# Kernel optimization log

Hardware: AMD Instinct MI355X
Metric: run time of the kernel (lower is better)

The kernel has to match this reference:

```python
import jax, jax.numpy as jnp
import numpy as np

B, D, K, N = 32, 512, 64, 1024
EPS = 1e-12  # torch F.normalize eps


def setup_inputs() -> dict:
    key = jax.random.key(0)
    k1, k2, k3 = jax.random.split(key, 3)
    x = jax.random.normal(k1, (B, D, N), dtype=jnp.float32)
    conv_w = jax.random.normal(k2, (K, D), dtype=jnp.float32) * (1.0 / np.sqrt(D))
    centers = jax.random.normal(k3, (D, K), dtype=jnp.float32)
    return {"x": x, "conv_w": conv_w, "centers": centers}


def reference(x, conv_w, centers):
    # scores: 1x1 conv over flattened spatial dim -> [B, K, N]
    scores = jnp.einsum('kd,bdn->bkn', conv_w, x)
    assign = jax.nn.softmax(scores, axis=1)                 # softmax over clusters
    # Algebraic rewrite of sum_n assign[b,k,n] * (x[b,d,n] - centers[d,k]):
    vlad = (jnp.einsum('bdn,bkn->bdk', x, assign)
            - centers[None, :, :] * assign.sum(axis=-1)[:, None, :])  # [B, D, K]
    # intra-normalization over descriptor dim D (F.normalize with eps clamp)
    vlad = vlad / jnp.maximum(jnp.linalg.norm(vlad, axis=1, keepdims=True), EPS)
    desc = vlad.reshape(vlad.shape[0], -1)                  # [B, D*K]
    desc = desc / jnp.maximum(jnp.linalg.norm(desc, axis=1, keepdims=True), EPS)
    return desc
```

## Files before the change

### kernel.cpp

```cpp
#include <hip/hip_runtime.h>
#include <hip/hip_bf16.h>

#define Bv 32
#define Dv 512
#define Kv 64
#define Nv 1024
#define EPSv 1e-12f

typedef __attribute__((ext_vector_type(8))) short bf16x8;
typedef __attribute__((ext_vector_type(4))) float f32x4;

__device__ __forceinline__ unsigned short f2b(float f) {
  union { float f; unsigned u; } v; v.f = f;
  unsigned r = v.u + 0x7fffu + ((v.u >> 16) & 1u);
  return (unsigned short)(r >> 16);
}
__device__ __forceinline__ unsigned pack2(float a, float b) {
  return (unsigned)f2b(a) | ((unsigned)f2b(b) << 16);
}

__global__ __launch_bounds__(256) void wconv(const float* __restrict__ w,
                                             unsigned short* __restrict__ wbf) {
  int i = (blockIdx.x * 256 + threadIdx.x) * 4;
  float4 v = *(const float4*)&w[i];
  uint2 o = make_uint2(pack2(v.x, v.y), pack2(v.z, v.w));
  *(uint2*)&wbf[i] = o;
}

__global__ __launch_bounds__(512) void fused_scores(
    const float* __restrict__ x, const unsigned short* __restrict__ wbf,
    unsigned short* __restrict__ xbf, unsigned short* __restrict__ assign,
    float* __restrict__ asum) {
  __shared__ unsigned short xT[64 * 520];
  __shared__ float redmax[4][64];
  __shared__ float redsum[4][64];

  const int t = threadIdx.x;
  const int b = blockIdx.y;
  const int n0 = blockIdx.x * 64;

  {
    const int lo = t & 15;
    const int hi = t >> 4;
    const float* xb = x + (size_t)b * Dv * Nv + n0;
    unsigned short* xo = xbf + (size_t)b * Dv * Nv + n0;
#pragma unroll
    for (int r = 0; r < 8; r++) {
      int d = (hi + 32 * r) * 2;
      int n4 = lo * 4;
      float4 v0 = *(const float4*)&xb[(size_t)d * Nv + n4];
      float4 v1 = *(const float4*)&xb[(size_t)(d + 1) * Nv + n4];
      unsigned short a0 = f2b(v0.x), a1 = f2b(v0.y), a2 = f2b(v0.z), a3 = f2b(v0.w);
      unsigned short b0 = f2b(v1.x), b1 = f2b(v1.y), b2 = f2b(v1.z), b3 = f2b(v1.w);
      *(uint2*)&xo[(size_t)d * Nv + n4] =
          make_uint2((unsigned)a0 | ((unsigned)a1 << 16), (unsigned)a2 | ((unsigned)a3 << 16));
      *(uint2*)&xo[(size_t)(d + 1) * Nv + n4] =
          make_uint2((unsigned)b0 | ((unsigned)b1 << 16), (unsigned)b2 | ((unsigned)b3 << 16));
      *(unsigned*)&xT[(n4 + 0) * 520 + d] = (unsigned)a0 | ((unsigned)b0 << 16);
      *(unsigned*)&xT[(n4 + 1) * 520 + d] = (unsigned)a1 | ((unsigned)b1 << 16);
      *(unsigned*)&xT[(n4 + 2) * 520 + d] = (unsigned)a2 | ((unsigned)b2 << 16);
      *(unsigned*)&xT[(n4 + 3) * 520 + d] = (unsigned)a3 | ((unsigned)b3 << 16);
    }
  }
  __syncthreads();

  const int wv = t >> 6;
  const int lane = t & 63;
  const int q = lane >> 4;
  const int m = lane & 15;
  const int k16 = wv & 3;
  const int nsub = wv >> 2;

  f32x4 acc0 = {0.f, 0.f, 0.f, 0.f};
  f32x4 acc1 = {0.f, 0.f, 0.f, 0.f};

  const unsigned short* wp = wbf + (size_t)(k16 * 16 + m) * Dv + q * 8;
  const unsigned short* l0 = &xT[(nsub * 32 + m) * 520 + q * 8];
  const unsigned short* l1 = l0 + 16 * 520;

#pragma unroll
  for (int d0 = 0; d0 < Dv; d0 += 32) {
    bf16x8 af = *(const bf16x8*)(wp + d0);
    bf16x8 bf0 = *(const bf16x8*)(l0 + d0);
    bf16x8 bf1 = *(const bf16x8*)(l1 + d0);
    acc0 = __builtin_amdgcn_mfma_f32_16x16x32_bf16(af, bf0, acc0, 0, 0, 0);
    acc1 = __builtin_amdgcn_mfma_f32_16x16x32_bf16(af, bf1, acc1, 0, 0, 0);
  }

  float m0 = fmaxf(fmaxf(acc0[0], acc0[1]), fmaxf(acc0[2], acc0[3]));
  float m1 = fmaxf(fmaxf(acc1[0], acc1[1]), fmaxf(acc1[2], acc1[3]));
  m0 = fmaxf(m0, __shfl_xor(m0, 16)); m0 = fmaxf(m0, __shfl_xor(m0, 32));
  m1 = fmaxf(m1, __shfl_xor(m1, 16)); m1 = fmaxf(m1, __shfl_xor(m1, 32));
  if (q == 0) {
    redmax[k16][nsub * 32 + m] = m0;
    redmax[k16][nsub * 32 + 16 + m] = m1;
  }
  __syncthreads();
  const int c0 = nsub * 32 + m, c1 = c0 + 16;
  float mc0 = fmaxf(fmaxf(redmax[0][c0], redmax[1][c0]), fmaxf(redmax[2][c0], redmax[3][c0]));
  float mc1 = fmaxf(fmaxf(redmax[0][c1], redmax[1][c1]), fmaxf(redmax[2][c1], redmax[3][c1]));

  float e0[4], e1[4];
  float s0 = 0.f, s1 = 0.f;
#pragma unroll
  for (int r = 0; r < 4; r++) {
    e0[r] = __expf(acc0[r] - mc0); s0 += e0[r];
    e1[r] = __expf(acc1[r] - mc1); s1 += e1[r];
  }
  s0 += __shfl_xor(s0, 16); s0 += __shfl_xor(s0, 32);
  s1 += __shfl_xor(s1, 16); s1 += __shfl_xor(s1, 32);
  if (q == 0) {
    redsum[k16][c0] = s0;
    redsum[k16][c1] = s1;
  }
  __syncthreads();
  float sc0 = 1.0f / (redsum[0][c0] + redsum[1][c0] + redsum[2][c0] + redsum[3][c0]);
  float sc1 = 1.0f / (redsum[0][c1] + redsum[1][c1] + redsum[2][c1] + redsum[3][c1]);

  unsigned short* ab = assign + ((size_t)b * Kv + k16 * 16 + q * 4) * Nv + n0 + nsub * 32;
#pragma unroll
  for (int r = 0; r < 4; r++) {
    float v0 = e0[r] * sc0;
    float v1 = e1[r] * sc1;
    ab[(size_t)r * Nv + m] = f2b(v0);
    ab[(size_t)r * Nv + 16 + m] = f2b(v1);
    float p = v0 + v1;
    p += __shfl_xor(p, 1); p += __shfl_xor(p, 2);
    p += __shfl_xor(p, 4); p += __shfl_xor(p, 8);
    if (m == 0) atomicAdd(&asum[b * Kv + k16 * 16 + q * 4 + r], p);
  }
}

__global__ __launch_bounds__(256) void vlad_mfma(
    const unsigned short* __restrict__ xbf, const unsigned short* __restrict__ assign,
    const float* __restrict__ centers, const float* __restrict__ asum,
    float* __restrict__ vlad, float* __restrict__ colsq) {
  __shared__ float sred[2][64][4];

  const int t = threadIdx.x;
  const int b = blockIdx.y;
  const int gx = blockIdx.x;
  const int d0 = (gx >> 1) * 16;
  const int kb = (gx & 1) * 32;
  const int wv = t >> 6;
  const int ksub = wv & 1;
  const int nh = wv >> 1;
  const int lane = t & 63;
  const int q = lane >> 4;
  const int m = lane & 15;
  const int k16 = kb + ksub * 16;

  f32x4 acc0 = {0.f, 0.f, 0.f, 0.f};
  f32x4 acc1 = {0.f, 0.f, 0.f, 0.f};

  const unsigned short* xp = xbf + ((size_t)b * Dv + d0 + m) * Nv + nh * 512 + q * 8;
  const unsigned short* ap = assign + ((size_t)b * Kv + k16 + m) * Nv + nh * 512 + q * 8;

#pragma unroll
  for (int n = 0; n < 512; n += 64) {
    bf16x8 a0 = *(const bf16x8*)(xp + n);
    bf16x8 f0 = *(const bf16x8*)(ap + n);
    bf16x8 a1 = *(const bf16x8*)(xp + n + 32);
    bf16x8 f1 = *(const bf16x8*)(ap + n + 32);
    acc0 = __builtin_amdgcn_mfma_f32_16x16x32_bf16(a0, f0, acc0, 0, 0, 0);
    acc1 = __builtin_amdgcn_mfma_f32_16x16x32_bf16(a1, f1, acc1, 0, 0, 0);
  }

  f32x4 v;
#pragma unroll
  for (int r = 0; r < 4; r++) v[r] = acc0[r] + acc1[r];

  if (nh == 1) {
#pragma unroll
    for (int r = 0; r < 4; r++) sred[ksub][lane][r] = v[r];
  }
  __syncthreads();
  if (nh == 0) {
    const int k = k16 + m;
    const float as = asum[b * Kv + k];
    float ss = 0.f;
#pragma unroll
    for (int r = 0; r < 4; r++) {
      v[r] += sred[ksub][lane][r];
      int d = d0 + q * 4 + r;
      float val = v[r] - centers[d * Kv + k] * as;
      vlad[((size_t)b * Dv + d) * Kv + k] = val;
      ss = fmaf(val, val, ss);
    }
    ss += __shfl_xor(ss, 16);
    ss += __shfl_xor(ss, 32);
    if (q == 0) atomicAdd(&colsq[b * Kv + k], ss);
  }
}

__global__ __launch_bounds__(256) void scale_kernel(
    const float* __restrict__ vlad, const float* __restrict__ colsq,
    float* __restrict__ out) {
  const int t = threadIdx.x;
  const size_t i = (size_t)blockIdx.x * 256 + t;
  const int b = (int)(i >> 15);
  __shared__ float scs[64];
  __shared__ float bsh;
  if (t < 64) {
    float tot = colsq[b * Kv + t];
    float sc = 1.0f / fmaxf(sqrtf(tot), EPSv);
    scs[t] = sc;
    float contrib = tot * sc * sc;
#pragma unroll
    for (int off = 32; off > 0; off >>= 1) contrib += __shfl_down(contrib, off);
    if (t == 0) bsh = 1.0f / fmaxf(sqrtf(contrib), EPSv);
  }
  __syncthreads();
  out[i] = vlad[i] * scs[i & 63] * bsh;
}

extern "C" void kernel_launch(void* const* d_in, const int* in_sizes, int n_in,
                              void* d_out, int out_size, void* d_ws, size_t ws_size,
                              hipStream_t stream) {
  const float* x = (const float*)d_in[0];
  const float* w = (const float*)d_in[1];
  const float* centers = (const float*)d_in[2];
  float* out = (float*)d_out;

  char* ws = (char*)d_ws;
  unsigned short* xbf = (unsigned short*)ws;
  unsigned short* assign = (unsigned short*)(ws + 33554432);
  float* vlad = (float*)(ws + 37748736);
  unsigned short* wbf = (unsigned short*)(ws + 41943040);
  float* asum = (float*)(ws + 42008576);
  float* colsq = asum + Bv * Kv;

  hipMemsetAsync(asum, 0, (size_t)2 * Bv * Kv * sizeof(float), stream);

  wconv<<<32, 256, 0, stream>>>(w, wbf);
  fused_scores<<<dim3(Nv / 64, Bv), 512, 0, stream>>>(x, wbf, xbf, assign, asum);
  vlad_mfma<<<dim3(64, Bv), 256, 0, stream>>>(xbf, assign, centers, asum, vlad, colsq);
  scale_kernel<<<(Bv * Dv * Kv) / 256, 256, 0, stream>>>(vlad, colsq, out);
}
```

Measured before the change: 147.6 us.

## Drop bf16 copy of x; convert fp32 x on the fly in both kernels

The scores kernel no longer writes a bf16 copy of x to global memory. The vlad kernel now reads the fp32 x directly and converts it to bf16 in registers before the MFMA. The scores kernel stages x through LDS in two halves of D, so its LDS tile is about half the size, which may allow higher occupancy. This removes a 32 MB write and replaces a 32 MB bf16 read with a 64 MB fp32 read that may partly hit in cache, at the cost of extra conversion ALU work and an extra barrier pair.

```diff
diff --git a/kernel.cpp b/kernel.cpp
--- a/kernel.cpp
+++ b/kernel.cpp
@@ -29,62 +29,53 @@
 
 __global__ __launch_bounds__(512) void fused_scores(
     const float* __restrict__ x, const unsigned short* __restrict__ wbf,
-    unsigned short* __restrict__ xbf, unsigned short* __restrict__ assign,
-    float* __restrict__ asum) {
-  __shared__ unsigned short xT[64 * 520];
+    unsigned short* __restrict__ assign, float* __restrict__ asum) {
+  __shared__ unsigned short xT[64 * 264];
   __shared__ float redmax[4][64];
   __shared__ float redsum[4][64];
 
   const int t = threadIdx.x;
   const int b = blockIdx.y;
   const int n0 = blockIdx.x * 64;
-
-  {
-    const int lo = t & 15;
-    const int hi = t >> 4;
-    const float* xb = x + (size_t)b * Dv * Nv + n0;
-    unsigned short* xo = xbf + (size_t)b * Dv * Nv + n0;
-#pragma unroll
-    for (int r = 0; r < 8; r++) {
-      int d = (hi + 32 * r) * 2;
-      int n4 = lo * 4;
-      float4 v0 = *(const float4*)&xb[(size_t)d * Nv + n4];
-      float4 v1 = *(const float4*)&xb[(size_t)(d + 1) * Nv + n4];
-      unsigned short a0 = f2b(v0.x), a1 = f2b(v0.y), a2 = f2b(v0.z), a3 = f2b(v0.w);
-      unsigned short b0 = f2b(v1.x), b1 = f2b(v1.y), b2 = f2b(v1.z), b3 = f2b(v1.w);
-      *(uint2*)&xo[(size_t)d * Nv + n4] =
-          make_uint2((unsigned)a0 | ((unsigned)a1 << 16), (unsigned)a2 | ((unsigned)a3 << 16));
-      *(uint2*)&xo[(size_t)(d + 1) * Nv + n4] =
-          make_uint2((unsigned)b0 | ((unsigned)b1 << 16), (unsigned)b2 | ((unsigned)b3 << 16));
-      *(unsigned*)&xT[(n4 + 0) * 520 + d] = (unsigned)a0 | ((unsigned)b0 << 16);
-      *(unsigned*)&xT[(n4 + 1) * 520 + d] = (unsigned)a1 | ((unsigned)b1 << 16);
-      *(unsigned*)&xT[(n4 + 2) * 520 + d] = (unsigned)a2 | ((unsigned)b2 << 16);
-      *(unsigned*)&xT[(n4 + 3) * 520 + d] = (unsigned)a3 | ((unsigned)b3 << 16);
-    }
-  }
-  __syncthreads();
-
   const int wv = t >> 6;
   const int lane = t & 63;
   const int q = lane >> 4;
   const int m = lane & 15;
   const int k16 = wv & 3;
   const int nsub = wv >> 2;
+  const int lo = t & 15;
+  const int hi = t >> 4;
 
   f32x4 acc0 = {0.f, 0.f, 0.f, 0.f};
   f32x4 acc1 = {0.f, 0.f, 0.f, 0.f};
 
   const unsigned short* wp = wbf + (size_t)(k16 * 16 + m) * Dv + q * 8;
-  const unsigned short* l0 = &xT[(nsub * 32 + m) * 520 + q * 8];
-  const unsigned short* l1 = l0 + 16 * 520;
-
-#pragma unroll
-  for (int d0 = 0; d0 < Dv; d0 += 32) {
-    bf16x8 af = *(const bf16x8*)(wp + d0);
-    bf16x8 bf0 = *(const bf16x8*)(l0 + d0);
-    bf16x8 bf1 = *(const bf16x8*)(l1 + d0);
-    acc0 = __builtin_amdgcn_mfma_f32_16x16x32_bf16(af, bf0, acc0, 0, 0, 0);
-    acc1 = __builtin_amdgcn_mfma_f32_16x16x32_bf16(af, bf1, acc1, 0, 0, 0);
+  const unsigned short* l0 = &xT[(nsub * 32 + m) * 264 + q * 8];
+  const unsigned short* l1 = l0 + 16 * 264;
+
+  for (int dh = 0; dh < 2; dh++) {
+    const float* xb = x + ((size_t)b * Dv + dh * 256) * Nv + n0;
+#pragma unroll
+    for (int r = 0; r < 4; r++) {
+      int d = (hi + 32 * r) * 2;
+      int n4 = lo * 4;
+      float4 v0 = *(const float4*)&xb[(size_t)d * Nv + n4];
+      float4 v1 = *(const float4*)&xb[(size_t)(d + 1) * Nv + n4];
+      *(unsigned*)&xT[(n4 + 0) * 264 + d] = pack2(v0.x, v1.x);
+      *(unsigned*)&xT[(n4 + 1) * 264 + d] = pack2(v0.y, v1.y);
+      *(unsigned*)&xT[(n4 + 2) * 264 + d] = pack2(v0.z, v1.z);
+      *(unsigned*)&xT[(n4 + 3) * 264 + d] = pack2(v0.w, v1.w);
+    }
+    __syncthreads();
+#pragma unroll
+    for (int d0 = 0; d0 < 256; d0 += 32) {
+      bf16x8 af = *(const bf16x8*)(wp + dh * 256 + d0);
+      bf16x8 bf0 = *(const bf16x8*)(l0 + d0);
+      bf16x8 bf1 = *(const bf16x8*)(l1 + d0);
+      acc0 = __builtin_amdgcn_mfma_f32_16x16x32_bf16(af, bf0, acc0, 0, 0, 0);
+      acc1 = __builtin_amdgcn_mfma_f32_16x16x32_bf16(af, bf1, acc1, 0, 0, 0);
+    }
+    __syncthreads();
   }
 
   float m0 = fmaxf(fmaxf(acc0[0], acc0[1]), fmaxf(acc0[2], acc0[3]));
@@ -132,7 +123,7 @@
 }
 
 __global__ __launch_bounds__(256) void vlad_mfma(
-    const unsigned short* __restrict__ xbf, const unsigned short* __restrict__ assign,
+    const float* __restrict__ x, const unsigned short* __restrict__ assign,
     const float* __restrict__ centers, const float* __restrict__ asum,
     float* __restrict__ vlad, float* __restrict__ colsq) {
   __shared__ float sred[2][64][4];
@@ -153,15 +144,26 @@
   f32x4 acc0 = {0.f, 0.f, 0.f, 0.f};
   f32x4 acc1 = {0.f, 0.f, 0.f, 0.f};
 
-  const unsigned short* xp = xbf + ((size_t)b * Dv + d0 + m) * Nv + nh * 512 + q * 8;
+  const float* xp = x + ((size_t)b * Dv + d0 + m) * Nv + nh * 512 + q * 8;
   const unsigned short* ap = assign + ((size_t)b * Kv + k16 + m) * Nv + nh * 512 + q * 8;
 
-#pragma unroll
+#pragma unroll 4
   for (int n = 0; n < 512; n += 64) {
-    bf16x8 a0 = *(const bf16x8*)(xp + n);
+    float4 xa0 = *(const float4*)(xp + n);
+    float4 xc0 = *(const float4*)(xp + n + 4);
     bf16x8 f0 = *(const bf16x8*)(ap + n);
-    bf16x8 a1 = *(const bf16x8*)(xp + n + 32);
+    float4 xa1 = *(const float4*)(xp + n + 32);
+    float4 xc1 = *(const float4*)(xp + n + 36);
     bf16x8 f1 = *(const bf16x8*)(ap + n + 32);
+    bf16x8 a0, a1;
+    a0[0] = (short)f2b(xa0.x); a0[1] = (short)f2b(xa0.y);
+    a0[2] = (short)f2b(xa0.z); a0[3] = (short)f2b(xa0.w);
+    a0[4] = (short)f2b(xc0.x); a0[5] = (short)f2b(xc0.y);
+    a0[6] = (short)f2b(xc0.z); a0[7] = (short)f2b(xc0.w);
+    a1[0] = (short)f2b(xa1.x); a1[1] = (short)f2b(xa1.y);
+    a1[2] = (short)f2b(xa1.z); a1[3] = (short)f2b(xa1.w);
+    a1[4] = (short)f2b(xc1.x); a1[5] = (short)f2b(xc1.y);
+    a1[6] = (short)f2b(xc1.z); a1[7] = (short)f2b(xc1.w);
     acc0 = __builtin_amdgcn_mfma_f32_16x16x32_bf16(a0, f0, acc0, 0, 0, 0);
     acc1 = __builtin_amdgcn_mfma_f32_16x16x32_bf16(a1, f1, acc1, 0, 0, 0);
   }
@@ -223,17 +225,16 @@
   float* out = (float*)d_out;
 
   char* ws = (char*)d_ws;
-  unsigned short* xbf = (unsigned short*)ws;
-  unsigned short* assign = (unsigned short*)(ws + 33554432);
-  float* vlad = (float*)(ws + 37748736);
-  unsigned short* wbf = (unsigned short*)(ws + 41943040);
-  float* asum = (float*)(ws + 42008576);
+  unsigned short* assign = (unsigned short*)ws;
+  float* vlad = (float*)(ws + 4194304);
+  unsigned short* wbf = (unsigned short*)(ws + 8388608);
+  float* asum = (float*)(ws + 8454144);
   float* colsq = asum + Bv * Kv;
 
   hipMemsetAsync(asum, 0, (size_t)2 * Bv * Kv * sizeof(float), stream);
 
   wconv<<<32, 256, 0, stream>>>(w, wbf);
-  fused_scores<<<dim3(Nv / 64, Bv), 512, 0, stream>>>(x, wbf, xbf, assign, asum);
-  vlad_mfma<<<dim3(64, Bv), 256, 0, stream>>>(xbf, assign, centers, asum, vlad, colsq);
+  fused_scores<<<dim3(Nv / 64, Bv), 512, 0, stream>>>(x, wbf, assign, asum);
+  vlad_mfma<<<dim3(64, Bv), 256, 0, stream>>>(x, assign, centers, asum, vlad, colsq);
   scale_kernel<<<(Bv * Dv * Kv) / 256, 256, 0, stream>>>(vlad, colsq, out);
 }
```

After: 157.6 us. 1.07x slower.

## Shrink score tiles, drop asum atomics, compute cluster sums inside vlad kernel

Applied to the files above, without the earlier changes.

The scores kernel now handles 32 spatial columns per block instead of 64. That doubles the grid and halves shared memory per block, which should raise occupancy. The per-cluster assignment sum is no longer built with atomics in the scores kernel. Instead the vlad kernel recomputes it from the bf16 assignment fragments it already loads, and each of its blocks covers all 64 clusters with 8 waves. This removes the atomic traffic and part of the memset, at the cost of extra conversion adds in the vlad inner loop and a sum taken from rounded bf16 values.

```diff
diff --git a/kernel.cpp b/kernel.cpp
--- a/kernel.cpp
+++ b/kernel.cpp
@@ -17,6 +17,9 @@
 }
 __device__ __forceinline__ unsigned pack2(float a, float b) {
   return (unsigned)f2b(a) | ((unsigned)f2b(b) << 16);
+}
+__device__ __forceinline__ float b2f(unsigned short s) {
+  union { unsigned u; float f; } v; v.u = (unsigned)s << 16; return v.f;
 }
 
 __global__ __launch_bounds__(256) void wconv(const float* __restrict__ w,
@@ -29,37 +32,34 @@
 
 __global__ __launch_bounds__(512) void fused_scores(
     const float* __restrict__ x, const unsigned short* __restrict__ wbf,
-    unsigned short* __restrict__ xbf, unsigned short* __restrict__ assign,
-    float* __restrict__ asum) {
-  __shared__ unsigned short xT[64 * 520];
-  __shared__ float redmax[4][64];
-  __shared__ float redsum[4][64];
+    unsigned short* __restrict__ xbf, unsigned short* __restrict__ assign) {
+  __shared__ unsigned short xT[32 * 520];
+  __shared__ float redmax[4][32];
+  __shared__ float redsum[4][32];
 
   const int t = threadIdx.x;
   const int b = blockIdx.y;
-  const int n0 = blockIdx.x * 64;
+  const int n0 = blockIdx.x * 32;
 
   {
-    const int lo = t & 15;
-    const int hi = t >> 4;
+    const int lo = t & 7;
+    const int hi = t >> 3;
     const float* xb = x + (size_t)b * Dv * Nv + n0;
     unsigned short* xo = xbf + (size_t)b * Dv * Nv + n0;
 #pragma unroll
-    for (int r = 0; r < 8; r++) {
-      int d = (hi + 32 * r) * 2;
+    for (int r = 0; r < 4; r++) {
+      int d = (hi + 64 * r) * 2;
       int n4 = lo * 4;
       float4 v0 = *(const float4*)&xb[(size_t)d * Nv + n4];
       float4 v1 = *(const float4*)&xb[(size_t)(d + 1) * Nv + n4];
-      unsigned short a0 = f2b(v0.x), a1 = f2b(v0.y), a2 = f2b(v0.z), a3 = f2b(v0.w);
-      unsigned short b0 = f2b(v1.x), b1 = f2b(v1.y), b2 = f2b(v1.z), b3 = f2b(v1.w);
       *(uint2*)&xo[(size_t)d * Nv + n4] =
-          make_uint2((unsigned)a0 | ((unsigned)a1 << 16), (unsigned)a2 | ((unsigned)a3 << 16));
+          make_uint2(pack2(v0.x, v0.y), pack2(v0.z, v0.w));
       *(uint2*)&xo[(size_t)(d + 1) * Nv + n4] =
-          make_uint2((unsigned)b0 | ((unsigned)b1 << 16), (unsigned)b2 | ((unsigned)b3 << 16));
-      *(unsigned*)&xT[(n4 + 0) * 520 + d] = (unsigned)a0 | ((unsigned)b0 << 16);
-      *(unsigned*)&xT[(n4 + 1) * 520 + d] = (unsigned)a1 | ((unsigned)b1 << 16);
-      *(unsigned*)&xT[(n4 + 2) * 520 + d] = (unsigned)a2 | ((unsigned)b2 << 16);
-      *(unsigned*)&xT[(n4 + 3) * 520 + d] = (unsigned)a3 | ((unsigned)b3 << 16);
+          make_uint2(pack2(v1.x, v1.y), pack2(v1.z, v1.w));
+      *(unsigned*)&xT[(n4 + 0) * 520 + d] = pack2(v0.x, v1.x);
+      *(unsigned*)&xT[(n4 + 1) * 520 + d] = pack2(v0.y, v1.y);
+      *(unsigned*)&xT[(n4 + 2) * 520 + d] = pack2(v0.z, v1.z);
+      *(unsigned*)&xT[(n4 + 3) * 520 + d] = pack2(v0.w, v1.w);
     }
   }
   __syncthreads();
@@ -71,119 +71,91 @@
   const int k16 = wv & 3;
   const int nsub = wv >> 2;
 
-  f32x4 acc0 = {0.f, 0.f, 0.f, 0.f};
-  f32x4 acc1 = {0.f, 0.f, 0.f, 0.f};
-
+  f32x4 acc = {0.f, 0.f, 0.f, 0.f};
   const unsigned short* wp = wbf + (size_t)(k16 * 16 + m) * Dv + q * 8;
-  const unsigned short* l0 = &xT[(nsub * 32 + m) * 520 + q * 8];
-  const unsigned short* l1 = l0 + 16 * 520;
+  const unsigned short* lp = &xT[(nsub * 16 + m) * 520 + q * 8];
 
 #pragma unroll
   for (int d0 = 0; d0 < Dv; d0 += 32) {
     bf16x8 af = *(const bf16x8*)(wp + d0);
-    bf16x8 bf0 = *(const bf16x8*)(l0 + d0);
-    bf16x8 bf1 = *(const bf16x8*)(l1 + d0);
-    acc0 = __builtin_amdgcn_mfma_f32_16x16x32_bf16(af, bf0, acc0, 0, 0, 0);
-    acc1 = __builtin_amdgcn_mfma_f32_16x16x32_bf16(af, bf1, acc1, 0, 0, 0);
-  }
-
-  float m0 = fmaxf(fmaxf(acc0[0], acc0[1]), fmaxf(acc0[2], acc0[3]));
-  float m1 = fmaxf(fmaxf(acc1[0], acc1[1]), fmaxf(acc1[2], acc1[3]));
-  m0 = fmaxf(m0, __shfl_xor(m0, 16)); m0 = fmaxf(m0, __shfl_xor(m0, 32));
-  m1 = fmaxf(m1, __shfl_xor(m1, 16)); m1 = fmaxf(m1, __shfl_xor(m1, 32));
-  if (q == 0) {
-    redmax[k16][nsub * 32 + m] = m0;
-    redmax[k16][nsub * 32 + 16 + m] = m1;
-  }
-  __syncthreads();
-  const int c0 = nsub * 32 + m, c1 = c0 + 16;
-  float mc0 = fmaxf(fmaxf(redmax[0][c0], redmax[1][c0]), fmaxf(redmax[2][c0], redmax[3][c0]));
-  float mc1 = fmaxf(fmaxf(redmax[0][c1], redmax[1][c1]), fmaxf(redmax[2][c1], redmax[3][c1]));
-
-  float e0[4], e1[4];
-  float s0 = 0.f, s1 = 0.f;
-#pragma unroll
-  for (int r = 0; r < 4; r++) {
-    e0[r] = __expf(acc0[r] - mc0); s0 += e0[r];
-    e1[r] = __expf(acc1[r] - mc1); s1 += e1[r];
-  }
-  s0 += __shfl_xor(s0, 16); s0 += __shfl_xor(s0, 32);
-  s1 += __shfl_xor(s1, 16); s1 += __shfl_xor(s1, 32);
-  if (q == 0) {
-    redsum[k16][c0] = s0;
-    redsum[k16][c1] = s1;
-  }
-  __syncthreads();
-  float sc0 = 1.0f / (redsum[0][c0] + redsum[1][c0] + redsum[2][c0] + redsum[3][c0]);
-  float sc1 = 1.0f / (redsum[0][c1] + redsum[1][c1] + redsum[2][c1] + redsum[3][c1]);
-
-  unsigned short* ab = assign + ((size_t)b * Kv + k16 * 16 + q * 4) * Nv + n0 + nsub * 32;
-#pragma unroll
-  for (int r = 0; r < 4; r++) {
-    float v0 = e0[r] * sc0;
-    float v1 = e1[r] * sc1;
-    ab[(size_t)r * Nv + m] = f2b(v0);
-    ab[(size_t)r * Nv + 16 + m] = f2b(v1);
-    float p = v0 + v1;
-    p += __shfl_xor(p, 1); p += __shfl_xor(p, 2);
-    p += __shfl_xor(p, 4); p += __shfl_xor(p, 8);
-    if (m == 0) atomicAdd(&asum[b * Kv + k16 * 16 + q * 4 + r], p);
-  }
-}
-
-__global__ __launch_bounds__(256) void vlad_mfma(
+    bf16x8 bf = *(const bf16x8*)(lp + d0);
+    acc = __builtin_amdgcn_mfma_f32_16x16x32_bf16(af, bf, acc, 0, 0, 0);
+  }
+
+  float mx = fmaxf(fmaxf(acc[0], acc[1]), fmaxf(acc[2], acc[3]));
+  mx = fmaxf(mx, __shfl_xor(mx, 16));
+  mx = fmaxf(mx, __shfl_xor(mx, 32));
+  if (q == 0) redmax[k16][nsub * 16 + m] = mx;
+  __syncthreads();
+  const int c = nsub * 16 + m;
+  float mc = fmaxf(fmaxf(redmax[0][c], redmax[1][c]),
+                   fmaxf(redmax[2][c], redmax[3][c]));
+  float e[4];
+  float s = 0.f;
+#pragma unroll
+  for (int r = 0; r < 4; r++) { e[r] = __expf(acc[r] - mc); s += e[r]; }
+  s += __shfl_xor(s, 16);
+  s += __shfl_xor(s, 32);
+  if (q == 0) redsum[k16][c] = s;
+  __syncthreads();
+  float sc = 1.0f / (redsum[0][c] + redsum[1][c] + redsum[2][c] + redsum[3][c]);
+
+  unsigned short* ab = assign + ((size_t)b * Kv + k16 * 16 + q * 4) * Nv + n0 + nsub * 16;
+#pragma unroll
+  for (int r = 0; r < 4; r++) ab[(size_t)r * Nv + m] = f2b(e[r] * sc);
+}
+
+__global__ __launch_bounds__(512) void vlad_mfma(
     const unsigned short* __restrict__ xbf, const unsigned short* __restrict__ assign,
-    const float* __restrict__ centers, const float* __restrict__ asum,
-    float* __restrict__ vlad, float* __restrict__ colsq) {
-  __shared__ float sred[2][64][4];
+    const float* __restrict__ centers, float* __restrict__ vlad,
+    float* __restrict__ colsq) {
+  __shared__ float sred[4][64][4];
+  __shared__ float sasum[4][16];
 
   const int t = threadIdx.x;
   const int b = blockIdx.y;
-  const int gx = blockIdx.x;
-  const int d0 = (gx >> 1) * 16;
-  const int kb = (gx & 1) * 32;
+  const int d0 = blockIdx.x * 16;
   const int wv = t >> 6;
-  const int ksub = wv & 1;
-  const int nh = wv >> 1;
+  const int ksub = wv & 3;
+  const int nh = wv >> 2;
   const int lane = t & 63;
   const int q = lane >> 4;
   const int m = lane & 15;
-  const int k16 = kb + ksub * 16;
-
-  f32x4 acc0 = {0.f, 0.f, 0.f, 0.f};
-  f32x4 acc1 = {0.f, 0.f, 0.f, 0.f};
+  const int k16 = ksub * 16;
+
+  f32x4 acc = {0.f, 0.f, 0.f, 0.f};
+  float sa = 0.f;
 
   const unsigned short* xp = xbf + ((size_t)b * Dv + d0 + m) * Nv + nh * 512 + q * 8;
   const unsigned short* ap = assign + ((size_t)b * Kv + k16 + m) * Nv + nh * 512 + q * 8;
 
 #pragma unroll
-  for (int n = 0; n < 512; n += 64) {
+  for (int n = 0; n < 512; n += 32) {
     bf16x8 a0 = *(const bf16x8*)(xp + n);
     bf16x8 f0 = *(const bf16x8*)(ap + n);
-    bf16x8 a1 = *(const bf16x8*)(xp + n + 32);
-    bf16x8 f1 = *(const bf16x8*)(ap + n + 32);
-    acc0 = __builtin_amdgcn_mfma_f32_16x16x32_bf16(a0, f0, acc0, 0, 0, 0);
-    acc1 = __builtin_amdgcn_mfma_f32_16x16x32_bf16(a1, f1, acc1, 0, 0, 0);
-  }
-
-  f32x4 v;
-#pragma unroll
-  for (int r = 0; r < 4; r++) v[r] = acc0[r] + acc1[r];
+    acc = __builtin_amdgcn_mfma_f32_16x16x32_bf16(a0, f0, acc, 0, 0, 0);
+#pragma unroll
+    for (int j = 0; j < 8; j++) sa += b2f((unsigned short)f0[j]);
+  }
+
+  sa += __shfl_xor(sa, 16);
+  sa += __shfl_xor(sa, 32);
 
   if (nh == 1) {
 #pragma unroll
-    for (int r = 0; r < 4; r++) sred[ksub][lane][r] = v[r];
+    for (int r = 0; r < 4; r++) sred[ksub][lane][r] = acc[r];
+    if (q == 0) sasum[ksub][m] = sa;
   }
   __syncthreads();
   if (nh == 0) {
     const int k = k16 + m;
-    const float as = asum[b * Kv + k];
+    const float asum_k = sa + sasum[ksub][m];
     float ss = 0.f;
 #pragma unroll
     for (int r = 0; r < 4; r++) {
-      v[r] += sred[ksub][lane][r];
+      float v = acc[r] + sred[ksub][lane][r];
       int d = d0 + q * 4 + r;
-      float val = v[r] - centers[d * Kv + k] * as;
+      float val = v - centers[d * Kv + k] * asum_k;
       vlad[((size_t)b * Dv + d) * Kv + k] = val;
       ss = fmaf(val, val, ss);
     }
@@ -223,17 +195,16 @@
   float* out = (float*)d_out;
 
   char* ws = (char*)d_ws;
-  unsigned short* xbf = (unsigned short*)ws;
-  unsigned short* assign = (unsigned short*)(ws + 33554432);
-  float* vlad = (float*)(ws + 37748736);
+  unsigned short* assign = (unsigned short*)ws;
+  float* vlad = (float*)(ws + 4194304);
+  unsigned short* xbf = (unsigned short*)(ws + 8388608);
   unsigned short* wbf = (unsigned short*)(ws + 41943040);
-  float* asum = (float*)(ws + 42008576);
-  float* colsq = asum + Bv * Kv;
-
-  hipMemsetAsync(asum, 0, (size_t)2 * Bv * Kv * sizeof(float), stream);
+  float* colsq = (float*)(ws + 42008576);
+
+  hipMemsetAsync(colsq, 0, (size_t)Bv * Kv * sizeof(float), stream);
 
   wconv<<<32, 256, 0, stream>>>(w, wbf);
-  fused_scores<<<dim3(Nv / 64, Bv), 512, 0, stream>>>(x, wbf, xbf, assign, asum);
-  vlad_mfma<<<dim3(64, Bv), 256, 0, stream>>>(xbf, assign, centers, asum, vlad, colsq);
+  fused_scores<<<dim3(Nv / 32, Bv), 512, 0, stream>>>(x, wbf, xbf, assign);
+  vlad_mfma<<<dim3(Dv / 16, Bv), 512, 0, stream>>>(xbf, assign, centers, vlad, colsq);
   scale_kernel<<<(Bv * Dv * Kv) / 256, 256, 0, stream>>>(vlad, colsq, out);
 }
```

Result: slower. 156.6 us (+6.1%).

## Widen vlad blocks to cover all clusters and batch loads ahead of MFMA

Applied to the files above, without the earlier changes.

vlad_mfma now uses 512-thread blocks that cover all 64 clusters for a 16-row slice of D, so each x tile is read by one block instead of two. Each wave issues all eight load pairs up front and refills them while the first batch of MFMAs runs, which is meant to hide global-load latency. The workspace is reordered so assign and vlad come before the large bf16 x buffer, and the bf16 packing in fused_scores now goes through pack2. The trade-off is higher register pressure from the 16 bf16x8 load registers, and the grid has half as many blocks.

```diff
diff --git a/kernel.cpp b/kernel.cpp
--- a/kernel.cpp
+++ b/kernel.cpp
@@ -50,16 +50,14 @@
       int n4 = lo * 4;
       float4 v0 = *(const float4*)&xb[(size_t)d * Nv + n4];
       float4 v1 = *(const float4*)&xb[(size_t)(d + 1) * Nv + n4];
-      unsigned short a0 = f2b(v0.x), a1 = f2b(v0.y), a2 = f2b(v0.z), a3 = f2b(v0.w);
-      unsigned short b0 = f2b(v1.x), b1 = f2b(v1.y), b2 = f2b(v1.z), b3 = f2b(v1.w);
       *(uint2*)&xo[(size_t)d * Nv + n4] =
-          make_uint2((unsigned)a0 | ((unsigned)a1 << 16), (unsigned)a2 | ((unsigned)a3 << 16));
+          make_uint2(pack2(v0.x, v0.y), pack2(v0.z, v0.w));
       *(uint2*)&xo[(size_t)(d + 1) * Nv + n4] =
-          make_uint2((unsigned)b0 | ((unsigned)b1 << 16), (unsigned)b2 | ((unsigned)b3 << 16));
-      *(unsigned*)&xT[(n4 + 0) * 520 + d] = (unsigned)a0 | ((unsigned)b0 << 16);
-      *(unsigned*)&xT[(n4 + 1) * 520 + d] = (unsigned)a1 | ((unsigned)b1 << 16);
-      *(unsigned*)&xT[(n4 + 2) * 520 + d] = (unsigned)a2 | ((unsigned)b2 << 16);
-      *(unsigned*)&xT[(n4 + 3) * 520 + d] = (unsigned)a3 | ((unsigned)b3 << 16);
+          make_uint2(pack2(v1.x, v1.y), pack2(v1.z, v1.w));
+      *(unsigned*)&xT[(n4 + 0) * 520 + d] = pack2(v0.x, v1.x);
+      *(unsigned*)&xT[(n4 + 1) * 520 + d] = pack2(v0.y, v1.y);
+      *(unsigned*)&xT[(n4 + 2) * 520 + d] = pack2(v0.z, v1.z);
+      *(unsigned*)&xT[(n4 + 3) * 520 + d] = pack2(v0.w, v1.w);
     }
   }
   __syncthreads();
@@ -131,48 +129,46 @@
   }
 }
 
-__global__ __launch_bounds__(256) void vlad_mfma(
+__global__ __launch_bounds__(512, 4) void vlad_mfma(
     const unsigned short* __restrict__ xbf, const unsigned short* __restrict__ assign,
     const float* __restrict__ centers, const float* __restrict__ asum,
     float* __restrict__ vlad, float* __restrict__ colsq) {
-  __shared__ float sred[2][64][4];
+  __shared__ float sred[4][64][4];
 
   const int t = threadIdx.x;
   const int b = blockIdx.y;
-  const int gx = blockIdx.x;
-  const int d0 = (gx >> 1) * 16;
-  const int kb = (gx & 1) * 32;
+  const int d0 = blockIdx.x * 16;
   const int wv = t >> 6;
-  const int ksub = wv & 1;
-  const int nh = wv >> 1;
+  const int ksub = wv & 3;
+  const int nh = wv >> 2;
   const int lane = t & 63;
   const int q = lane >> 4;
   const int m = lane & 15;
-  const int k16 = kb + ksub * 16;
-
-  f32x4 acc0 = {0.f, 0.f, 0.f, 0.f};
-  f32x4 acc1 = {0.f, 0.f, 0.f, 0.f};
+  const int k16 = ksub * 16;
 
   const unsigned short* xp = xbf + ((size_t)b * Dv + d0 + m) * Nv + nh * 512 + q * 8;
   const unsigned short* ap = assign + ((size_t)b * Kv + k16 + m) * Nv + nh * 512 + q * 8;
 
-#pragma unroll
-  for (int n = 0; n < 512; n += 64) {
-    bf16x8 a0 = *(const bf16x8*)(xp + n);
-    bf16x8 f0 = *(const bf16x8*)(ap + n);
-    bf16x8 a1 = *(const bf16x8*)(xp + n + 32);
-    bf16x8 f1 = *(const bf16x8*)(ap + n + 32);
-    acc0 = __builtin_amdgcn_mfma_f32_16x16x32_bf16(a0, f0, acc0, 0, 0, 0);
-    acc1 = __builtin_amdgcn_mfma_f32_16x16x32_bf16(a1, f1, acc1, 0, 0, 0);
-  }
-
-  f32x4 v;
-#pragma unroll
-  for (int r = 0; r < 4; r++) v[r] = acc0[r] + acc1[r];
+  f32x4 acc = {0.f, 0.f, 0.f, 0.f};
+  bf16x8 xv[8], av[8];
+#pragma unroll
+  for (int i = 0; i < 8; i++) {
+    xv[i] = *(const bf16x8*)(xp + i * 32);
+    av[i] = *(const bf16x8*)(ap + i * 32);
+  }
+#pragma unroll
+  for (int i = 0; i < 8; i++) {
+    acc = __builtin_amdgcn_mfma_f32_16x16x32_bf16(xv[i], av[i], acc, 0, 0, 0);
+    xv[i] = *(const bf16x8*)(xp + 256 + i * 32);
+    av[i] = *(const bf16x8*)(ap + 256 + i * 32);
+  }
+#pragma unroll
+  for (int i = 0; i < 8; i++)
+    acc = __builtin_amdgcn_mfma_f32_16x16x32_bf16(xv[i], av[i], acc, 0, 0, 0);
 
   if (nh == 1) {
 #pragma unroll
-    for (int r = 0; r < 4; r++) sred[ksub][lane][r] = v[r];
+    for (int r = 0; r < 4; r++) sred[ksub][lane][r] = acc[r];
   }
   __syncthreads();
   if (nh == 0) {
@@ -181,9 +177,9 @@
     float ss = 0.f;
 #pragma unroll
     for (int r = 0; r < 4; r++) {
-      v[r] += sred[ksub][lane][r];
+      float v = acc[r] + sred[ksub][lane][r];
       int d = d0 + q * 4 + r;
-      float val = v[r] - centers[d * Kv + k] * as;
+      float val = v - centers[d * Kv + k] * as;
       vlad[((size_t)b * Dv + d) * Kv + k] = val;
       ss = fmaf(val, val, ss);
     }
@@ -223,9 +219,9 @@
   float* out = (float*)d_out;
 
   char* ws = (char*)d_ws;
-  unsigned short* xbf = (unsigned short*)ws;
-  unsigned short* assign = (unsigned short*)(ws + 33554432);
-  float* vlad = (float*)(ws + 37748736);
+  unsigned short* assign = (unsigned short*)ws;
+  float* vlad = (float*)(ws + 4194304);
+  unsigned short* xbf = (unsigned short*)(ws + 8388608);
   unsigned short* wbf = (unsigned short*)(ws + 41943040);
   float* asum = (float*)(ws + 42008576);
   float* colsq = asum + Bv * Kv;
@@ -234,6 +230,6 @@
 
   wconv<<<32, 256, 0, stream>>>(w, wbf);
   fused_scores<<<dim3(Nv / 64, Bv), 512, 0, stream>>>(x, wbf, xbf, assign, asum);
-  vlad_mfma<<<dim3(64, Bv), 256, 0, stream>>>(xbf, assign, centers, asum, vlad, colsq);
+  vlad_mfma<<<dim3(Dv / 16, Bv), 512, 0, stream>>>(xbf, assign, centers, asum, vlad, colsq);
   scale_kernel<<<(Bv * Dv * Kv) / 256, 256, 0, stream>>>(vlad, colsq, out);
 }
```

Result: no change. 147.4 us (-0.2%).
